# Optimization experiments

Measured on AMD Instinct MI355X. Metric: run time of the kernel, lower is better.

## Reference

```python
import jax, jax.numpy as jnp
import numpy as np

N = 50000   # nodes
E = 200000  # edges
C = 32      # conv_dim
ND = 75     # n_atom_features
ED = 12     # n_bond_features
L = 3       # num_layer
G = 500     # num graphs in batch
HID = 5     # neurons_message
EPS = 1e-5


def leaky(v):
    return jnp.where(v > 0, v, 0.01 * v)


def setup_inputs() -> dict:
    key = jax.random.key(0)
    ks = jax.random.split(key, 16)
    x = jax.random.normal(ks[0], (N, ND), jnp.float32)
    edge_index = jax.random.randint(ks[1], (2, E), 0, N, jnp.int32)
    edge_attr = jax.random.uniform(ks[2], (E, ED), jnp.float32)
    batch = jnp.sort(jax.random.randint(ks[3], (N,), 0, G, jnp.int32))
    return {
        "x": x,
        "edge_index": edge_index,
        "edge_attr": edge_attr,
        "batch": batch,
        "lin_W": jax.random.normal(ks[4], (ND, C), jnp.float32) * 0.1,
        "lin_b": jnp.zeros((C,), jnp.float32),
        "mes_W1": jax.random.normal(ks[5], (L, ED, HID), jnp.float32) * 0.3,
        "mes_b1": jnp.zeros((L, HID), jnp.float32),
        "mes_W2": jax.random.normal(ks[6], (L, HID, C * C), jnp.float32) * 0.05,
        "mes_b2": jnp.zeros((L, C * C), jnp.float32),
        "root_W": jax.random.normal(ks[7], (L, C, C), jnp.float32) * 0.1,
        "conv_b": jnp.zeros((L, C), jnp.float32),
        "bn_g": jnp.ones((L, C), jnp.float32),
        "bn_b": jnp.zeros((L, C), jnp.float32),
        "pred_W": jax.random.normal(ks[8], (C, 1), jnp.float32) * 0.1,
        "pred_b": jnp.zeros((1,), jnp.float32),
    }


def reference(x, edge_index, edge_attr, batch, lin_W, lin_b, mes_W1, mes_b1,
              mes_W2, mes_b2, root_W, conv_b, bn_g, bn_b, pred_W, pred_b):
    src, dst = edge_index[0], edge_index[1]
    # initial atom projection
    h = leaky(x @ lin_W + lin_b)  # [N, C]
    for l in range(L):
        # edge MLP -> per-edge weight matrix [E, C, C]
        w = jnp.maximum(edge_attr @ mes_W1[l] + mes_b1[l], 0.0)
        w = (w @ mes_W2[l] + mes_b2[l]).reshape(E, C, C)
        # gather source features, per-edge matmul, scatter-add to targets
        msg = jnp.einsum('ec,ecd->ed', h[src], w)  # [E, C]
        agg = jax.ops.segment_sum(msg, dst, num_segments=N)  # [N, C]
        out = agg + h @ root_W[l] + conv_b[l]
        # batch norm (batch statistics over nodes)
        mu = out.mean(axis=0)
        var = out.var(axis=0)
        out = (out - mu) / jnp.sqrt(var + EPS) * bn_g[l] + bn_b[l]
        if l < L - 1:
            out = leaky(out)
        h = out  # JK == 'last'
    # graph readout: scatter_add over batch ids, then prediction head
    g = jax.ops.segment_sum(h, batch, num_segments=G)  # [G, C]
    return g @ pred_W + pred_b  # [G, 1]
```

## Files before the change

### kernel.cpp

```cpp
#include <hip/hip_runtime.h>

namespace {

constexpr int kN = 50000, kE = 200000, kG = 500;
constexpr float kEps = 1e-5f;
constexpr int kNB = (kN + 255) / 256;
constexpr int kEB = (kE + 255) / 256;

typedef short v8s __attribute__((ext_vector_type(8)));
typedef float v4f __attribute__((ext_vector_type(4)));

struct U3 { unsigned a, b, c; };

__device__ __forceinline__ unsigned short bf16rn(float x) {
    unsigned u = __float_as_uint(x);
    return (unsigned short)((u + 0x7FFFu + ((u >> 16) & 1u)) >> 16);
}
__device__ __forceinline__ float bf16lo(unsigned p) { return __uint_as_float(p << 16); }
__device__ __forceinline__ float bf16hi(unsigned p) { return __uint_as_float(p & 0xFFFF0000u); }
__device__ __forceinline__ unsigned pk2(float a, float b) {
    return (unsigned)bf16rn(a) | ((unsigned)bf16rn(b) << 16);
}

__global__ __launch_bounds__(256) void deg_hist(
    const int* __restrict__ ei, int* __restrict__ deg)
{
    int e = blockIdx.x * 256 + threadIdx.x;
    if (e < kE) atomicAdd(&deg[ei[kE + e]], 1);
}

__global__ __launch_bounds__(1024) void init_h(
    const float* __restrict__ x, const float* __restrict__ W,
    const float* __restrict__ b, float* __restrict__ hbuf,
    int* __restrict__ deg, float* __restrict__ stats)
{
    __shared__ unsigned short sx[256 * 96];
    __shared__ unsigned short sW[32 * 96];
    int t = threadIdx.x;
    {
        int z = blockIdx.x * 256 + t;
        if (t < 256 && z < kN) deg[z] = 0;
        if (blockIdx.x == 0) for (int i = t; i < 1536; i += 1024) stats[i] = 0.f;
    }
    for (int i = t; i < 256 * 96; i += 1024) sx[i] = 0;
    for (int i = t; i < 32 * 96; i += 1024) sW[i] = 0;
    __syncthreads();
    int tb = blockIdx.x * 256;
    int cnt = min(256, kN - tb);
    for (int i = t; i < cnt * 75; i += 1024) {
        int n = i / 75, f = i - n * 75;
        sx[n * 96 + f] = bf16rn(x[(size_t)tb * 75 + i]);
    }
    for (int i = t; i < 75 * 32; i += 1024) {
        int f = i >> 5, c = i & 31;
        sW[c * 96 + f] = bf16rn(W[i]);
    }
    __syncthreads();
    int l15 = t & 15, quad = (t >> 4) & 3, w = t >> 6;
    #pragma unroll
    for (int tile = 0; tile < 2; ++tile) {
        v4f acc = {0.f, 0.f, 0.f, 0.f};
        #pragma unroll
        for (int kc = 0; kc < 3; ++kc) {
            v8s a  = *(const v8s*)&sx[(w * 16 + l15) * 96 + kc * 32 + quad * 8];
            v8s bb = *(const v8s*)&sW[(tile * 16 + l15) * 96 + kc * 32 + quad * 8];
            acc = __builtin_amdgcn_mfma_f32_16x16x32_bf16(a, bb, acc, 0, 0, 0);
        }
        int c = tile * 16 + l15;
        float bc = b[c];
        #pragma unroll
        for (int r = 0; r < 4; ++r) {
            int n = tb + w * 16 + quad * 4 + r;
            if (n < kN) {
                float v = acc[r] + bc;
                hbuf[(size_t)n * 32 + c] = v > 0.f ? v : 0.01f * v;
            }
        }
    }
}

__global__ __launch_bounds__(256) void scan_part(
    const int* __restrict__ deg, int* __restrict__ blkSum)
{
    __shared__ int sc[256];
    int t = threadIdx.x;
    int idx = blockIdx.x * 256 + t;
    sc[t] = (idx < kN) ? deg[idx] : 0;
    __syncthreads();
    #pragma unroll
    for (int off = 128; off > 0; off >>= 1) {
        if (t < off) sc[t] += sc[t + off];
        __syncthreads();
    }
    if (t == 0) blkSum[blockIdx.x] = sc[0];
}

__global__ __launch_bounds__(256) void scan_add(
    const int* __restrict__ deg, const int* __restrict__ blkSum,
    int* __restrict__ cursor)
{
    __shared__ int sc[256];
    __shared__ int sOff;
    int t = threadIdx.x;
    sc[t] = (t < blockIdx.x) ? blkSum[t] : 0;
    __syncthreads();
    #pragma unroll
    for (int off = 128; off > 0; off >>= 1) {
        if (t < off) sc[t] += sc[t + off];
        __syncthreads();
    }
    if (t == 0) sOff = sc[0];
    __syncthreads();
    int idx = blockIdx.x * 256 + t;
    int v = (idx < kN) ? deg[idx] : 0;
    sc[t] = v;
    __syncthreads();
    #pragma unroll
    for (int off = 1; off < 256; off <<= 1) {
        int u = (t >= off) ? sc[t - off] : 0;
        __syncthreads();
        sc[t] += u;
        __syncthreads();
    }
    if (idx < kN) cursor[idx] = sOff + sc[t] - v;
}

__global__ __launch_bounds__(256) void hid_pre(
    const float* __restrict__ ea, const float* __restrict__ W1,
    const float* __restrict__ b1, const int* __restrict__ ei,
    int* __restrict__ cursor, uint4* __restrict__ hq)
{
    __shared__ float sE[256 * 13];
    __shared__ float sW[195];
    int t = threadIdx.x;
    for (int i = t; i < 195; i += 256) sW[i] = (i < 180) ? W1[i] : b1[i - 180];
    int base = blockIdx.x * 256;
    int cnt = min(256, kE - base);
    for (int i = t; i < cnt * 12; i += 256) {
        int el = i / 12, f = i - el * 12;
        sE[el * 13 + f] = ea[(size_t)base * 12 + i];
    }
    __syncthreads();
    if (t >= cnt) return;
    int e = base + t;
    unsigned src = (unsigned)ei[e];
    unsigned dst = (unsigned)ei[kE + e];
    int pos = atomicAdd(&cursor[dst], 1);
    float ef[12];
    #pragma unroll
    for (int j = 0; j < 12; ++j) ef[j] = sE[t * 13 + j];
    #pragma unroll
    for (int l = 0; l < 3; ++l) {
        float h[5];
        #pragma unroll
        for (int k = 0; k < 5; ++k) h[k] = sW[180 + l * 5 + k];
        #pragma unroll
        for (int f = 0; f < 12; ++f)
            #pragma unroll
            for (int k = 0; k < 5; ++k)
                h[k] = fmaf(ef[f], sW[l * 60 + f * 5 + k], h[k]);
        #pragma unroll
        for (int k = 0; k < 5; ++k) h[k] = h[k] > 0.f ? h[k] : 0.f;
        hq[(size_t)l * kE + pos] = make_uint4(
            pk2(h[0], h[1]), pk2(h[2], h[3]),
            (unsigned)bf16rn(h[4]) | (src << 16), dst);
    }
}

__global__ __launch_bounds__(1024) void y_root(
    const float* __restrict__ hbuf, float* __restrict__ obuf,
    const float* __restrict__ W2, const float* __restrict__ b2,
    const float* __restrict__ rW, const float* __restrict__ convb,
    const float* __restrict__ statsR,
    const float* __restrict__ gPrev, const float* __restrict__ bPrev,
    int first, unsigned* __restrict__ Ydw)
{
    __shared__ unsigned short sh[256 * 32];
    __shared__ unsigned short sB[256 * 32];
    int t = threadIdx.x;
    int tb = blockIdx.x * 256;
    int cnt = min(256, kN - tb);
    for (int i = t; i < 8192; i += 1024) {
        int co = i >> 5, c = i & 31, d = co >> 3, k = co & 7;
        float v = (k < 5) ? W2[k * 1024 + c * 32 + d]
                : (k == 5) ? b2[c * 32 + d]
                : (k == 6) ? rW[c * 32 + d] : 0.f;
        sB[co * 32 + c] = bf16rn(v);
    }
    if (first) {
        #pragma unroll
        for (int j = 0; j < 8; ++j) {
            int idx = t + j * 1024;
            int nl = idx >> 5, c = idx & 31;
            float v = (nl < cnt) ? hbuf[(size_t)(tb + nl) * 32 + c] : 0.f;
            sh[idx] = bf16rn(v);
        }
    } else {
        int c = t & 31;
        float sum = 0.f, sq = 0.f;
        #pragma unroll
        for (int r = 0; r < 8; ++r) {
            sum += statsR[r * 64 + c];
            sq  += statsR[r * 64 + 32 + c];
        }
        float mu = sum * (1.f / kN);
        float var = sq * (1.f / kN) - mu * mu;
        float ivg = rsqrtf(var + kEps) * gPrev[c];
        float bb = bPrev[c];
        #pragma unroll
        for (int j = 0; j < 8; ++j) {
            int idx = t + j * 1024;
            int nl = idx >> 5;
            float v = 0.f;
            if (nl < cnt) {
                float o = obuf[(size_t)(tb + nl) * 32 + c];
                v = (o - mu) * ivg + bb;
                v = v > 0.f ? v : 0.01f * v;
            }
            sh[idx] = bf16rn(v);
        }
    }
    __syncthreads();
    int l15 = t & 15, quad = (t >> 4) & 3, w = t >> 6;
    int n = tb + w * 16 + l15;
    v8s bn_ = *(const v8s*)&sh[(w * 16 + l15) * 32 + quad * 8];
    #pragma unroll
    for (int i = 0; i < 16; ++i) {
        v8s a = *(const v8s*)&sB[(i * 16 + l15) * 32 + quad * 8];
        v4f acc = {0.f, 0.f, 0.f, 0.f};
        acc = __builtin_amdgcn_mfma_f32_16x16x32_bf16(a, bn_, acc, 0, 0, 0);
        if (n < kN) {
            int cb = i * 16 + quad * 4;
            int d = cb >> 3, koff = cb & 7;
            if (koff == 0) {
                Ydw[(size_t)n * 96 + d * 3]     = pk2(acc[0], acc[1]);
                Ydw[(size_t)n * 96 + d * 3 + 1] = pk2(acc[2], acc[3]);
            } else {
                Ydw[(size_t)n * 96 + d * 3 + 2] = pk2(acc[0], acc[1]);
                obuf[(size_t)n * 32 + d] = acc[2] + convb[d];
            }
        }
    }
}

__global__ __launch_bounds__(256) void edge_scat(
    const uint4* __restrict__ hq, const unsigned* __restrict__ Ydw,
    float* __restrict__ obuf)
{
    int gid = blockIdx.x * 256 + threadIdx.x;
    int grp = gid >> 5;
    int d = gid & 31;
    int e0 = grp * 8;
    uint4 q0 = hq[e0],     q1 = hq[e0 + 1], q2 = hq[e0 + 2], q3 = hq[e0 + 3];
    uint4 q4 = hq[e0 + 4], q5 = hq[e0 + 5], q6 = hq[e0 + 6], q7 = hq[e0 + 7];
    U3 P0 = *(const U3*)(Ydw + ((q0.z >> 16) * 96u + d * 3u));
    U3 P1 = *(const U3*)(Ydw + ((q1.z >> 16) * 96u + d * 3u));
    U3 P2 = *(const U3*)(Ydw + ((q2.z >> 16) * 96u + d * 3u));
    U3 P3 = *(const U3*)(Ydw + ((q3.z >> 16) * 96u + d * 3u));
    U3 P4 = *(const U3*)(Ydw + ((q4.z >> 16) * 96u + d * 3u));
    U3 P5 = *(const U3*)(Ydw + ((q5.z >> 16) * 96u + d * 3u));
    U3 P6 = *(const U3*)(Ydw + ((q6.z >> 16) * 96u + d * 3u));
    U3 P7 = *(const U3*)(Ydw + ((q7.z >> 16) * 96u + d * 3u));
    float m0 = bf16hi(P0.c);
    m0 = fmaf(bf16lo(q0.x), bf16lo(P0.a), m0);
    m0 = fmaf(bf16hi(q0.x), bf16hi(P0.a), m0);
    m0 = fmaf(bf16lo(q0.y), bf16lo(P0.b), m0);
    m0 = fmaf(bf16hi(q0.y), bf16hi(P0.b), m0);
    m0 = fmaf(bf16lo(q0.z), bf16lo(P0.c), m0);
    float m1 = bf16hi(P1.c);
    m1 = fmaf(bf16lo(q1.x), bf16lo(P1.a), m1);
    m1 = fmaf(bf16hi(q1.x), bf16hi(P1.a), m1);
    m1 = fmaf(bf16lo(q1.y), bf16lo(P1.b), m1);
    m1 = fmaf(bf16hi(q1.y), bf16hi(P1.b), m1);
    m1 = fmaf(bf16lo(q1.z), bf16lo(P1.c), m1);
    float m2 = bf16hi(P2.c);
    m2 = fmaf(bf16lo(q2.x), bf16lo(P2.a), m2);
    m2 = fmaf(bf16hi(q2.x), bf16hi(P2.a), m2);
    m2 = fmaf(bf16lo(q2.y), bf16lo(P2.b), m2);
    m2 = fmaf(bf16hi(q2.y), bf16hi(P2.b), m2);
    m2 = fmaf(bf16lo(q2.z), bf16lo(P2.c), m2);
    float m3 = bf16hi(P3.c);
    m3 = fmaf(bf16lo(q3.x), bf16lo(P3.a), m3);
    m3 = fmaf(bf16hi(q3.x), bf16hi(P3.a), m3);
    m3 = fmaf(bf16lo(q3.y), bf16lo(P3.b), m3);
    m3 = fmaf(bf16hi(q3.y), bf16hi(P3.b), m3);
    m3 = fmaf(bf16lo(q3.z), bf16lo(P3.c), m3);
    float m4 = bf16hi(P4.c);
    m4 = fmaf(bf16lo(q4.x), bf16lo(P4.a), m4);
    m4 = fmaf(bf16hi(q4.x), bf16hi(P4.a), m4);
    m4 = fmaf(bf16lo(q4.y), bf16lo(P4.b), m4);
    m4 = fmaf(bf16hi(q4.y), bf16hi(P4.b), m4);
    m4 = fmaf(bf16lo(q4.z), bf16lo(P4.c), m4);
    float m5 = bf16hi(P5.c);
    m5 = fmaf(bf16lo(q5.x), bf16lo(P5.a), m5);
    m5 = fmaf(bf16hi(q5.x), bf16hi(P5.a), m5);
    m5 = fmaf(bf16lo(q5.y), bf16lo(P5.b), m5);
    m5 = fmaf(bf16hi(q5.y), bf16hi(P5.b), m5);
    m5 = fmaf(bf16lo(q5.z), bf16lo(P5.c), m5);
    float m6 = bf16hi(P6.c);
    m6 = fmaf(bf16lo(q6.x), bf16lo(P6.a), m6);
    m6 = fmaf(bf16hi(q6.x), bf16hi(P6.a), m6);
    m6 = fmaf(bf16lo(q6.y), bf16lo(P6.b), m6);
    m6 = fmaf(bf16hi(q6.y), bf16hi(P6.b), m6);
    m6 = fmaf(bf16lo(q6.z), bf16lo(P6.c), m6);
    float m7 = bf16hi(P7.c);
    m7 = fmaf(bf16lo(q7.x), bf16lo(P7.a), m7);
    m7 = fmaf(bf16hi(q7.x), bf16hi(P7.a), m7);
    m7 = fmaf(bf16lo(q7.y), bf16lo(P7.b), m7);
    m7 = fmaf(bf16hi(q7.y), bf16hi(P7.b), m7);
    m7 = fmaf(bf16lo(q7.z), bf16lo(P7.c), m7);
    float acc = m0;
    unsigned cur = q0.w;
    if (q1.w == cur) acc += m1;
    else { atomicAdd(&obuf[cur * 32u + d], acc); cur = q1.w; acc = m1; }
    if (q2.w == cur) acc += m2;
    else { atomicAdd(&obuf[cur * 32u + d], acc); cur = q2.w; acc = m2; }
    if (q3.w == cur) acc += m3;
    else { atomicAdd(&obuf[cur * 32u + d], acc); cur = q3.w; acc = m3; }
    if (q4.w == cur) acc += m4;
    else { atomicAdd(&obuf[cur * 32u + d], acc); cur = q4.w; acc = m4; }
    if (q5.w == cur) acc += m5;
    else { atomicAdd(&obuf[cur * 32u + d], acc); cur = q5.w; acc = m5; }
    if (q6.w == cur) acc += m6;
    else { atomicAdd(&obuf[cur * 32u + d], acc); cur = q6.w; acc = m6; }
    if (q7.w == cur) acc += m7;
    else { atomicAdd(&obuf[cur * 32u + d], acc); cur = q7.w; acc = m7; }
    atomicAdd(&obuf[cur * 32u + d], acc);
}

__global__ __launch_bounds__(256) void bn_reduce(
    const float* __restrict__ obuf, float* __restrict__ statsR,
    float* __restrict__ out, const float* __restrict__ pred_b, int last)
{
    __shared__ float ls[256];
    __shared__ float lq[256];
    int t = threadIdx.x;
    {
        int gi = blockIdx.x * 256 + t;
        if (last && gi < kG) out[gi] = pred_b[0];
    }
    int c = t & 31, row = t >> 5;
    float s = 0.f, q = 0.f;
    for (int n = blockIdx.x * 8 + row; n < kN; n += gridDim.x * 8) {
        float v = obuf[(size_t)n * 32 + c];
        s += v; q += v * v;
    }
    ls[t] = s; lq[t] = q;
    __syncthreads();
    if (t < 128) { ls[t] += ls[t + 128]; lq[t] += lq[t + 128]; }
    __syncthreads();
    if (t < 64) { ls[t] += ls[t + 64]; lq[t] += lq[t + 64]; }
    __syncthreads();
    if (t < 32) {
        float* rep = statsR + (blockIdx.x & 7) * 64;
        atomicAdd(&rep[t], ls[t] + ls[t + 32]);
        atomicAdd(&rep[32 + t], lq[t] + lq[t + 32]);
    }
}

__global__ __launch_bounds__(256) void bn_pred_readout(
    const float* __restrict__ obuf, const float* __restrict__ statsR,
    const float* __restrict__ g, const float* __restrict__ b,
    const float* __restrict__ predW, const int* __restrict__ batch,
    float* __restrict__ out)
{
    __shared__ float sv[8];
    __shared__ int sb[8];
    int t = threadIdx.x;
    int idx = blockIdx.x * 256 + t;
    int c = t & 31;
    int row = t >> 5;
    int n = idx >> 5;
    float sum = 0.f, sq = 0.f;
    #pragma unroll
    for (int r = 0; r < 8; ++r) {
        sum += statsR[r * 64 + c];
        sq  += statsR[r * 64 + 32 + c];
    }
    float mu = sum * (1.f / kN);
    float var = sq * (1.f / kN) - mu * mu;
    float inv = rsqrtf(var + kEps);
    float pv = 0.f;
    if (n < kN) {
        float v = (obuf[idx] - mu) * inv * g[c] + b[c];
        pv = v * predW[c];
    }
    #pragma unroll
    for (int off = 16; off > 0; off >>= 1) pv += __shfl_down(pv, off, 32);
    if (c == 0) { sv[row] = pv; sb[row] = (n < kN) ? batch[n] : -1; }
    __syncthreads();
    if (t == 0) {
        int cur = sb[0]; float acc = sv[0];
        #pragma unroll
        for (int i = 1; i < 8; ++i) {
            if (sb[i] == cur) acc += sv[i];
            else {
                if (cur >= 0) atomicAdd(&out[cur], acc);
                cur = sb[i]; acc = sv[i];
            }
        }
        if (cur >= 0) atomicAdd(&out[cur], acc);
    }
}

}

extern "C" void kernel_launch(void* const* d_in, const int* in_sizes, int n_in,
                              void* d_out, int out_size, void* d_ws, size_t ws_size,
                              hipStream_t stream)
{
    const float* x      = (const float*)d_in[0];
    const int*   ei     = (const int*)d_in[1];
    const float* ea     = (const float*)d_in[2];
    const int*   batch  = (const int*)d_in[3];
    const float* lin_W  = (const float*)d_in[4];
    const float* lin_b  = (const float*)d_in[5];
    const float* mes_W1 = (const float*)d_in[6];
    const float* mes_b1 = (const float*)d_in[7];
    const float* mes_W2 = (const float*)d_in[8];
    const float* mes_b2 = (const float*)d_in[9];
    const float* root_W = (const float*)d_in[10];
    const float* conv_b = (const float*)d_in[11];
    const float* bn_g   = (const float*)d_in[12];
    const float* bn_b   = (const float*)d_in[13];
    const float* pred_W = (const float*)d_in[14];
    const float* pred_b = (const float*)d_in[15];
    float* out = (float*)d_out;

    char* wsb = (char*)d_ws;
    float* stats = (float*)wsb;
    int* deg     = (int*)(wsb + 8192);
    int* cursor  = deg + kN;
    int* blkSum  = cursor + kN;
    float* hbuf  = (float*)(blkSum + 256);
    float* obuf  = hbuf + (size_t)kN * 32;
    unsigned short* Yus = (unsigned short*)(obuf + (size_t)kN * 32);
    unsigned* Ydw = (unsigned*)Yus;
    uint4* hq    = (uint4*)(Yus + (size_t)kN * 192);

    init_h<<<kNB, 1024, 0, stream>>>(x, lin_W, lin_b, hbuf, deg, stats);
    deg_hist<<<kEB, 256, 0, stream>>>(ei, deg);
    scan_part<<<kNB, 256, 0, stream>>>(deg, blkSum);
    scan_add<<<kNB, 256, 0, stream>>>(deg, blkSum, cursor);
    hid_pre<<<kEB, 256, 0, stream>>>(ea, mes_W1, mes_b1, ei, cursor, hq);

    int scatBlocks = (kE / 8) * 32 / 256;
    for (int l = 0; l < 3; ++l) {
        y_root<<<kNB, 1024, 0, stream>>>(
            hbuf, obuf, mes_W2 + (size_t)l * 5120, mes_b2 + (size_t)l * 1024,
            root_W + (size_t)l * 1024, conv_b + l * 32,
            stats + (l ? (l - 1) * 512 : 0),
            bn_g + (l ? (l - 1) * 32 : 0), bn_b + (l ? (l - 1) * 32 : 0),
            l == 0 ? 1 : 0, Ydw);
        edge_scat<<<scatBlocks, 256, 0, stream>>>(
            hq + (size_t)l * kE, Ydw, obuf);
        bn_reduce<<<512, 256, 0, stream>>>(obuf, stats + l * 512, out, pred_b,
                                           l == 2 ? 1 : 0);
    }

    bn_pred_readout<<<(kN * 32 + 255) / 256, 256, 0, stream>>>(
        obuf, stats + 2 * 512, bn_g + 64, bn_b + 64, pred_W, batch, out);
}
```

Measured before the change: 281.5 us.

## Stage y_root outputs in swizzled LDS and write coalesced vectors, smaller blocks

The y_root kernel now handles 64 nodes per 256-thread block instead of 256 nodes per 1024-thread block. MFMA results go to XOR-swizzled shared-memory staging buffers rather than being stored as scattered dword writes. A second pass then writes Ydw and obuf to global memory with contiguous 16-byte vector stores. Blocks now run on partial tiles without bounds checks, so the obuf and Y buffers are padded to a multiple of 64 nodes. The cost is that the 16 KB weight tile is reloaded and converted four times as often, and each block uses more LDS.

```diff
diff --git a/kernel.cpp b/kernel.cpp
--- a/kernel.cpp
+++ b/kernel.cpp
@@ -6,6 +6,8 @@
 constexpr float kEps = 1e-5f;
 constexpr int kNB = (kN + 255) / 256;
 constexpr int kEB = (kE + 255) / 256;
+constexpr int kNT = (kN + 63) / 64;
+constexpr int kNP = kNT * 64;
 
 typedef short v8s __attribute__((ext_vector_type(8)));
 typedef float v4f __attribute__((ext_vector_type(4)));
@@ -167,7 +169,7 @@
     }
 }
 
-__global__ __launch_bounds__(1024) void y_root(
+__global__ __launch_bounds__(256) void y_root(
     const float* __restrict__ hbuf, float* __restrict__ obuf,
     const float* __restrict__ W2, const float* __restrict__ b2,
     const float* __restrict__ rW, const float* __restrict__ convb,
@@ -175,27 +177,20 @@
     const float* __restrict__ gPrev, const float* __restrict__ bPrev,
     int first, unsigned* __restrict__ Ydw)
 {
-    __shared__ unsigned short sh[256 * 32];
     __shared__ unsigned short sB[256 * 32];
-    int t = threadIdx.x;
-    int tb = blockIdx.x * 256;
-    int cnt = min(256, kN - tb);
-    for (int i = t; i < 8192; i += 1024) {
+    __shared__ unsigned short sh[64 * 32];
+    __shared__ unsigned Yst[64 * 96];
+    __shared__ float OBst[64 * 32];
+    int t = threadIdx.x;
+    for (int i = t; i < 8192; i += 256) {
         int co = i >> 5, c = i & 31, d = co >> 3, k = co & 7;
         float v = (k < 5) ? W2[k * 1024 + c * 32 + d]
                 : (k == 5) ? b2[c * 32 + d]
                 : (k == 6) ? rW[c * 32 + d] : 0.f;
         sB[co * 32 + c] = bf16rn(v);
     }
-    if (first) {
-        #pragma unroll
-        for (int j = 0; j < 8; ++j) {
-            int idx = t + j * 1024;
-            int nl = idx >> 5, c = idx & 31;
-            float v = (nl < cnt) ? hbuf[(size_t)(tb + nl) * 32 + c] : 0.f;
-            sh[idx] = bf16rn(v);
-        }
-    } else {
+    float mu = 0.f, ivg = 0.f, bb = 0.f;
+    if (!first) {
         int c = t & 31;
         float sum = 0.f, sq = 0.f;
         #pragma unroll
@@ -203,17 +198,29 @@
             sum += statsR[r * 64 + c];
             sq  += statsR[r * 64 + 32 + c];
         }
-        float mu = sum * (1.f / kN);
+        mu = sum * (1.f / kN);
         float var = sq * (1.f / kN) - mu * mu;
-        float ivg = rsqrtf(var + kEps) * gPrev[c];
-        float bb = bPrev[c];
+        ivg = rsqrtf(var + kEps) * gPrev[c];
+        bb = bPrev[c];
+    }
+    int tb = blockIdx.x * 64;
+    int cnt = min(64, kN - tb);
+    if (first) {
         #pragma unroll
         for (int j = 0; j < 8; ++j) {
-            int idx = t + j * 1024;
+            int idx = t + j * 256;
+            int nl = idx >> 5;
+            float v = (nl < cnt) ? hbuf[(size_t)(tb + nl) * 32 + (idx & 31)] : 0.f;
+            sh[idx] = bf16rn(v);
+        }
+    } else {
+        #pragma unroll
+        for (int j = 0; j < 8; ++j) {
+            int idx = t + j * 256;
             int nl = idx >> 5;
             float v = 0.f;
             if (nl < cnt) {
-                float o = obuf[(size_t)(tb + nl) * 32 + c];
+                float o = obuf[(size_t)(tb + nl) * 32 + (t & 31)];
                 v = (o - mu) * ivg + bb;
                 v = v > 0.f ? v : 0.01f * v;
             }
@@ -222,24 +229,39 @@
     }
     __syncthreads();
     int l15 = t & 15, quad = (t >> 4) & 3, w = t >> 6;
-    int n = tb + w * 16 + l15;
-    v8s bn_ = *(const v8s*)&sh[(w * 16 + l15) * 32 + quad * 8];
+    int row = w * 16 + l15;
+    int sz = (row & 7) << 2;
+    v8s bn_ = *(const v8s*)&sh[row * 32 + quad * 8];
     #pragma unroll
     for (int i = 0; i < 16; ++i) {
         v8s a = *(const v8s*)&sB[(i * 16 + l15) * 32 + quad * 8];
         v4f acc = {0.f, 0.f, 0.f, 0.f};
         acc = __builtin_amdgcn_mfma_f32_16x16x32_bf16(a, bn_, acc, 0, 0, 0);
-        if (n < kN) {
-            int cb = i * 16 + quad * 4;
-            int d = cb >> 3, koff = cb & 7;
-            if (koff == 0) {
-                Ydw[(size_t)n * 96 + d * 3]     = pk2(acc[0], acc[1]);
-                Ydw[(size_t)n * 96 + d * 3 + 1] = pk2(acc[2], acc[3]);
-            } else {
-                Ydw[(size_t)n * 96 + d * 3 + 2] = pk2(acc[0], acc[1]);
-                obuf[(size_t)n * 32 + d] = acc[2] + convb[d];
-            }
-        }
+        int d = 2 * i + (quad >> 1);
+        if ((quad & 1) == 0) {
+            Yst[row * 96 + ((d * 3)     ^ sz)] = pk2(acc[0], acc[1]);
+            Yst[row * 96 + ((d * 3 + 1) ^ sz)] = pk2(acc[2], acc[3]);
+        } else {
+            Yst[row * 96 + ((d * 3 + 2) ^ sz)] = pk2(acc[0], acc[1]);
+            OBst[row * 32 + (d ^ sz)] = acc[2];
+        }
+    }
+    __syncthreads();
+    #pragma unroll
+    for (int j = 0; j < 6; ++j) {
+        int L = j * 1024 + t * 4;
+        int r2 = L / 96, c2 = L - r2 * 96;
+        uint4 v = *(const uint4*)&Yst[r2 * 96 + (c2 ^ ((r2 & 7) << 2))];
+        *(uint4*)&Ydw[(size_t)tb * 96 + L] = v;
+    }
+    float4 cbv = *(const float4*)&convb[(t & 7) * 4];
+    #pragma unroll
+    for (int j = 0; j < 2; ++j) {
+        int L = j * 1024 + t * 4;
+        int r2 = L >> 5, c2 = L & 31;
+        float4 v = *(const float4*)&OBst[r2 * 32 + (c2 ^ ((r2 & 7) << 2))];
+        v.x += cbv.x; v.y += cbv.y; v.z += cbv.z; v.w += cbv.w;
+        *(float4*)&obuf[(size_t)tb * 32 + L] = v;
     }
 }
 
@@ -434,9 +456,9 @@
     int* blkSum  = cursor + kN;
     float* hbuf  = (float*)(blkSum + 256);
     float* obuf  = hbuf + (size_t)kN * 32;
-    unsigned short* Yus = (unsigned short*)(obuf + (size_t)kN * 32);
+    unsigned short* Yus = (unsigned short*)(obuf + (size_t)kNP * 32);
     unsigned* Ydw = (unsigned*)Yus;
-    uint4* hq    = (uint4*)(Yus + (size_t)kN * 192);
+    uint4* hq    = (uint4*)(Yus + (size_t)kNP * 192);
 
     init_h<<<kNB, 1024, 0, stream>>>(x, lin_W, lin_b, hbuf, deg, stats);
     deg_hist<<<kEB, 256, 0, stream>>>(ei, deg);
@@ -446,7 +468,7 @@
 
     int scatBlocks = (kE / 8) * 32 / 256;
     for (int l = 0; l < 3; ++l) {
-        y_root<<<kNB, 1024, 0, stream>>>(
+        y_root<<<kNT, 256, 0, stream>>>(
             hbuf, obuf, mes_W2 + (size_t)l * 5120, mes_b2 + (size_t)l * 1024,
             root_W + (size_t)l * 1024, conv_b + l * 32,
             stats + (l ? (l - 1) * 512 : 0),
```

Result: slower. 310.3 us (+10.2%).

## Precompute bf16 weight tiles once and shrink y_root to LDS-free 64-node blocks

Applied to the files above, without the earlier changes.

The per-layer bf16 conversion of W2, b2 and root_W into the MFMA B-operand layout is moved into the deg_hist kernel, done once for all three layers and written to workspace. y_root no longer stages weights or node features through shared memory. Each thread loads its 8 node features directly, applies the batch-norm and leaky-ReLU with per-channel parameters fetched by shuffles, and reads weight fragments from global or L2. Blocks become 256 threads covering 64 nodes, which gives more blocks and removes the __syncthreads, at the cost of scattered global reads for the weights and the features.

```diff
diff --git a/kernel.cpp b/kernel.cpp
--- a/kernel.cpp
+++ b/kernel.cpp
@@ -6,6 +6,7 @@
 constexpr float kEps = 1e-5f;
 constexpr int kNB = (kN + 255) / 256;
 constexpr int kEB = (kE + 255) / 256;
+constexpr int kYB = (kN + 63) / 64;
 
 typedef short v8s __attribute__((ext_vector_type(8)));
 typedef float v4f __attribute__((ext_vector_type(4)));
@@ -23,10 +24,21 @@
 }
 
 __global__ __launch_bounds__(256) void deg_hist(
-    const int* __restrict__ ei, int* __restrict__ deg)
+    const int* __restrict__ ei, int* __restrict__ deg,
+    const float* __restrict__ W2all, const float* __restrict__ b2all,
+    const float* __restrict__ rWall, unsigned short* __restrict__ Wb)
 {
     int e = blockIdx.x * 256 + threadIdx.x;
     if (e < kE) atomicAdd(&deg[ei[kE + e]], 1);
+    if (e < 3 * 8192) {
+        int l = e >> 13, i = e & 8191;
+        int co = i >> 5, c = i & 31, d = co >> 3, k = co & 7;
+        const float* W2 = W2all + (size_t)l * 5120;
+        float v = (k < 5) ? W2[k * 1024 + c * 32 + d]
+                : (k == 5) ? b2all[(size_t)l * 1024 + c * 32 + d]
+                : (k == 6) ? rWall[(size_t)l * 1024 + c * 32 + d] : 0.f;
+        Wb[(size_t)l * 8192 + co * 32 + c] = bf16rn(v);
+    }
 }
 
 __global__ __launch_bounds__(1024) void init_h(
@@ -167,35 +179,19 @@
     }
 }
 
-__global__ __launch_bounds__(1024) void y_root(
+__global__ __launch_bounds__(256) void y_root(
     const float* __restrict__ hbuf, float* __restrict__ obuf,
-    const float* __restrict__ W2, const float* __restrict__ b2,
-    const float* __restrict__ rW, const float* __restrict__ convb,
+    const unsigned short* __restrict__ Wb, const float* __restrict__ convb,
     const float* __restrict__ statsR,
     const float* __restrict__ gPrev, const float* __restrict__ bPrev,
     int first, unsigned* __restrict__ Ydw)
 {
-    __shared__ unsigned short sh[256 * 32];
-    __shared__ unsigned short sB[256 * 32];
-    int t = threadIdx.x;
-    int tb = blockIdx.x * 256;
-    int cnt = min(256, kN - tb);
-    for (int i = t; i < 8192; i += 1024) {
-        int co = i >> 5, c = i & 31, d = co >> 3, k = co & 7;
-        float v = (k < 5) ? W2[k * 1024 + c * 32 + d]
-                : (k == 5) ? b2[c * 32 + d]
-                : (k == 6) ? rW[c * 32 + d] : 0.f;
-        sB[co * 32 + c] = bf16rn(v);
-    }
-    if (first) {
-        #pragma unroll
-        for (int j = 0; j < 8; ++j) {
-            int idx = t + j * 1024;
-            int nl = idx >> 5, c = idx & 31;
-            float v = (nl < cnt) ? hbuf[(size_t)(tb + nl) * 32 + c] : 0.f;
-            sh[idx] = bf16rn(v);
-        }
-    } else {
+    int t = threadIdx.x;
+    int l15 = t & 15, quad = (t >> 4) & 3, w = t >> 6;
+    int n = blockIdx.x * 64 + w * 16 + l15;
+    int c0 = quad * 8;
+    float muO = 0.f, ivgO = 0.f, bbO = 0.f;
+    if (!first) {
         int c = t & 31;
         float sum = 0.f, sq = 0.f;
         #pragma unroll
@@ -203,30 +199,33 @@
             sum += statsR[r * 64 + c];
             sq  += statsR[r * 64 + 32 + c];
         }
-        float mu = sum * (1.f / kN);
-        float var = sq * (1.f / kN) - mu * mu;
-        float ivg = rsqrtf(var + kEps) * gPrev[c];
-        float bb = bPrev[c];
-        #pragma unroll
-        for (int j = 0; j < 8; ++j) {
-            int idx = t + j * 1024;
-            int nl = idx >> 5;
-            float v = 0.f;
-            if (nl < cnt) {
-                float o = obuf[(size_t)(tb + nl) * 32 + c];
-                v = (o - mu) * ivg + bb;
+        float m = sum * (1.f / kN);
+        float var = sq * (1.f / kN) - m * m;
+        muO = m; ivgO = rsqrtf(var + kEps) * gPrev[c]; bbO = bPrev[c];
+    }
+    v8s bn_ = {0, 0, 0, 0, 0, 0, 0, 0};
+    if (n < kN) {
+        if (first) {
+            const float* hp = hbuf + (size_t)n * 32 + c0;
+            #pragma unroll
+            for (int j = 0; j < 8; ++j)
+                bn_[j] = (short)bf16rn(hp[j]);
+        } else {
+            const float* op = obuf + (size_t)n * 32 + c0;
+            #pragma unroll
+            for (int j = 0; j < 8; ++j) {
+                float m  = __shfl(muO,  c0 + j, 32);
+                float iv = __shfl(ivgO, c0 + j, 32);
+                float bv = __shfl(bbO,  c0 + j, 32);
+                float v = (op[j] - m) * iv + bv;
                 v = v > 0.f ? v : 0.01f * v;
+                bn_[j] = (short)bf16rn(v);
             }
-            sh[idx] = bf16rn(v);
-        }
-    }
-    __syncthreads();
-    int l15 = t & 15, quad = (t >> 4) & 3, w = t >> 6;
-    int n = tb + w * 16 + l15;
-    v8s bn_ = *(const v8s*)&sh[(w * 16 + l15) * 32 + quad * 8];
+        }
+    }
     #pragma unroll
     for (int i = 0; i < 16; ++i) {
-        v8s a = *(const v8s*)&sB[(i * 16 + l15) * 32 + quad * 8];
+        v8s a = *(const v8s*)&Wb[(i * 16 + l15) * 32 + c0];
         v4f acc = {0.f, 0.f, 0.f, 0.f};
         acc = __builtin_amdgcn_mfma_f32_16x16x32_bf16(a, bn_, acc, 0, 0, 0);
         if (n < kN) {
@@ -437,18 +436,18 @@
     unsigned short* Yus = (unsigned short*)(obuf + (size_t)kN * 32);
     unsigned* Ydw = (unsigned*)Yus;
     uint4* hq    = (uint4*)(Yus + (size_t)kN * 192);
+    unsigned short* Wb = (unsigned short*)(hq + (size_t)3 * kE);
 
     init_h<<<kNB, 1024, 0, stream>>>(x, lin_W, lin_b, hbuf, deg, stats);
-    deg_hist<<<kEB, 256, 0, stream>>>(ei, deg);
+    deg_hist<<<kEB, 256, 0, stream>>>(ei, deg, mes_W2, mes_b2, root_W, Wb);
     scan_part<<<kNB, 256, 0, stream>>>(deg, blkSum);
     scan_add<<<kNB, 256, 0, stream>>>(deg, blkSum, cursor);
     hid_pre<<<kEB, 256, 0, stream>>>(ea, mes_W1, mes_b1, ei, cursor, hq);
 
     int scatBlocks = (kE / 8) * 32 / 256;
     for (int l = 0; l < 3; ++l) {
-        y_root<<<kNB, 1024, 0, stream>>>(
-            hbuf, obuf, mes_W2 + (size_t)l * 5120, mes_b2 + (size_t)l * 1024,
-            root_W + (size_t)l * 1024, conv_b + l * 32,
+        y_root<<<kYB, 256, 0, stream>>>(
+            hbuf, obuf, Wb + (size_t)l * 8192, conv_b + l * 32,
             stats + (l ? (l - 1) * 512 : 0),
             bn_g + (l ? (l - 1) * 32 : 0), bn_b + (l ? (l - 1) * 32 : 0),
             l == 0 ? 1 : 0, Ydw);
```

Result: faster. 272.9 us, median of 2 (-3.0%).
